# Optimization experiments

Hardware: AMD Instinct MI355X
Metric: run time of the kernel (lower is better)

The kernel has to match this reference:

```python
import jax, jax.numpy as jnp
import numpy as np

KSIZE = 5  # per init_kwargs
NORMALIZATION = "sum"


def setup_inputs() -> dict:
    key = jax.random.key(0)
    k1, k2 = jax.random.split(key)
    kernel = jax.random.normal(k1, (8, KSIZE * KSIZE, 508, 508), dtype=jnp.float32)
    tensor = jax.random.normal(k2, (8, 3, 512, 512), dtype=jnp.float32)
    return {"kernel": kernel, "tensor": tensor}


def _apply_kernels(kernel, tensor, ksize=KSIZE, normalization=NORMALIZATION):
    # kernel: [bs, k*k, kh, kw], tensor: [bs, ci, h, w]
    kh, kw = kernel.shape[2], kernel.shape[3]
    bs, ci, h, w = tensor.shape
    needed = kh + ksize - 1
    if needed > h:
        crop = (needed - h) // 2
        if crop > 0:
            kernel = kernel[:, :, crop:-crop, crop:-crop]
        kh, kw = kernel.shape[2], kernel.shape[3]
    else:
        crop = (h - needed) // 2
        if crop > 0:
            tensor = tensor[:, :, crop:-crop, crop:-crop]
    # Per-pixel dynamic convolution: for each output pixel (i,j),
    # out[b,c,i,j] = sum_{di,dj} kernel[b, di*k+dj, i, j] * tensor[b, c, i+di, j+dj].
    # Loop over the k*k fixed taps (small, static) instead of materializing
    # the [bs, ci, kh, kw, k*k] unfolded tiles the torch code builds.
    weighted = jnp.zeros((bs, ci, kh, kw), dtype=tensor.dtype)
    for di in range(ksize):
        for dj in range(ksize):
            w_tap = kernel[:, di * ksize + dj][:, None]          # [bs,1,kh,kw]
            weighted = weighted + w_tap * tensor[:, :, di:di + kh, dj:dj + kw]
    if normalization == "sum":
        kernel_sum = jnp.sum(kernel, axis=1, keepdims=True)      # [bs,1,kh,kw]
    elif normalization == "l1":
        kernel_sum = jnp.sum(jnp.abs(kernel), axis=1, keepdims=True)
    else:
        kernel_sum = None
    return weighted, kernel_sum


def reference(kernel, tensor):
    return _apply_kernels(kernel, tensor)
```

## Files before the change

### kernel.cpp

```cpp
#include <hip/hip_runtime.h>


constexpr int BS = 8;
constexpr int CI = 3;
constexpr int KH = 508;
constexpr int KW = 508;
constexpr int TH = 512;
constexpr int TW = 512;
constexpr int KSZ = 5;
constexpr int KK = KSZ * KSZ;
constexpr int QPR = KW / 4;
constexpr long long KPLANE = (long long)KH * KW;
constexpr long long WOUT_SIZE = (long long)BS * CI * KPLANE;

__global__ __launch_bounds__(256) void apply_kernels_kern(
    const float* __restrict__ kern,
    const float* __restrict__ tens,
    float* __restrict__ out)
{
    int tid = blockIdx.x * 256 + threadIdx.x;
    if (tid >= BS * KH * QPR) return;
    int q = tid % QPR;
    int t = tid / QPR;
    int y = t % KH;
    int b = t / KH;
    int x = q * 4;

    const float* kbase = kern + (size_t)b * KK * KPLANE + (size_t)y * KW + x;
    const float* tbase = tens + (size_t)b * CI * TH * TW + (size_t)y * TW + x;

    float acc[CI][4] = {};
    float ksum[4] = {};

#pragma unroll
    for (int di = 0; di < KSZ; ++di) {
        float tr[CI][8];
#pragma unroll
        for (int c = 0; c < CI; ++c) {
            const float* tp = tbase + (size_t)c * TH * TW + (size_t)di * TW;
            const float4 a  = *(const float4*)(tp);
            const float4 b4 = *(const float4*)(tp + 4);
            tr[c][0] = a.x;  tr[c][1] = a.y;  tr[c][2] = a.z;  tr[c][3] = a.w;
            tr[c][4] = b4.x; tr[c][5] = b4.y; tr[c][6] = b4.z; tr[c][7] = b4.w;
        }
#pragma unroll
        for (int dj = 0; dj < KSZ; ++dj) {
            const float4 k4 = *(const float4*)(kbase + (size_t)(di * KSZ + dj) * KPLANE);
            const float kv[4] = {k4.x, k4.y, k4.z, k4.w};
#pragma unroll
            for (int l = 0; l < 4; ++l) {
                ksum[l] += kv[l];
#pragma unroll
                for (int c = 0; c < CI; ++c)
                    acc[c][l] += kv[l] * tr[c][l + dj];
            }
        }
    }

#pragma unroll
    for (int c = 0; c < CI; ++c) {
        float4 v = {acc[c][0], acc[c][1], acc[c][2], acc[c][3]};
        *(float4*)(out + ((size_t)(b * CI + c) * KH + y) * KW + x) = v;
    }
    float4 s = {ksum[0], ksum[1], ksum[2], ksum[3]};
    *(float4*)(out + WOUT_SIZE + ((size_t)b * KH + y) * KW + x) = s;
}

extern "C" void kernel_launch(void* const* d_in, const int* in_sizes, int n_in,
                              void* d_out, int out_size, void* d_ws, size_t ws_size,
                              hipStream_t stream) {
    const float* kern = (const float*)d_in[0];
    const float* tens = (const float*)d_in[1];
    float* out = (float*)d_out;
    const int total = BS * KH * QPR;
    const int blocks = (total + 255) / 256;
    apply_kernels_kern<<<blocks, 256, 0, stream>>>(kern, tens, out);
}
```

Measured before the change: 300.8 us.

## Compute two output rows per thread and use nontemporal kernel loads/stores

Each thread now produces outputs for two adjacent rows. It loads six tensor rows instead of ten, so tensor reads are shared across both rows. The per-pixel kernel weights and the outputs, which are streamed once, now go through nontemporal load and store builtins to avoid polluting the cache. This halves the thread count and raises register pressure per thread. The workload is dominated by the kernel-weight stream, which is unchanged in size.

```diff
diff --git a/kernel.cpp b/kernel.cpp
--- a/kernel.cpp
+++ b/kernel.cpp
@@ -10,8 +10,18 @@
 constexpr int KSZ = 5;
 constexpr int KK = KSZ * KSZ;
 constexpr int QPR = KW / 4;
+constexpr int YPAIRS = KH / 2;
 constexpr long long KPLANE = (long long)KH * KW;
 constexpr long long WOUT_SIZE = (long long)BS * CI * KPLANE;
+
+typedef float vf4 __attribute__((ext_vector_type(4)));
+
+__device__ __forceinline__ vf4 nt_load4(const float* p) {
+    return __builtin_nontemporal_load((const vf4*)p);
+}
+__device__ __forceinline__ void nt_store4(float* p, vf4 v) {
+    __builtin_nontemporal_store(v, (vf4*)p);
+}
 
 __global__ __launch_bounds__(256) void apply_kernels_kern(
     const float* __restrict__ kern,
@@ -19,51 +29,61 @@
     float* __restrict__ out)
 {
     int tid = blockIdx.x * 256 + threadIdx.x;
-    if (tid >= BS * KH * QPR) return;
+    if (tid >= BS * YPAIRS * QPR) return;
     int q = tid % QPR;
     int t = tid / QPR;
-    int y = t % KH;
-    int b = t / KH;
+    int yi = t % YPAIRS;
+    int b = t / YPAIRS;
+    int y0 = yi * 2;
     int x = q * 4;
 
-    const float* kbase = kern + (size_t)b * KK * KPLANE + (size_t)y * KW + x;
-    const float* tbase = tens + (size_t)b * CI * TH * TW + (size_t)y * TW + x;
+    const float* kbase = kern + (size_t)b * KK * KPLANE + (size_t)y0 * KW + x;
+    const float* tbase = tens + (size_t)b * CI * TH * TW + (size_t)y0 * TW + x;
 
-    float acc[CI][4] = {};
-    float ksum[4] = {};
+    float acc[2][CI][4] = {};
+    float ksum[2][4] = {};
 
 #pragma unroll
-    for (int di = 0; di < KSZ; ++di) {
-        float tr[CI][8];
+    for (int r = 0; r < KSZ + 1; ++r) {
+        float tw[CI][8];
 #pragma unroll
         for (int c = 0; c < CI; ++c) {
-            const float* tp = tbase + (size_t)c * TH * TW + (size_t)di * TW;
-            const float4 a  = *(const float4*)(tp);
-            const float4 b4 = *(const float4*)(tp + 4);
-            tr[c][0] = a.x;  tr[c][1] = a.y;  tr[c][2] = a.z;  tr[c][3] = a.w;
-            tr[c][4] = b4.x; tr[c][5] = b4.y; tr[c][6] = b4.z; tr[c][7] = b4.w;
+            const float* tp = tbase + (size_t)c * TH * TW + (size_t)r * TW;
+            const vf4 a  = *(const vf4*)(tp);
+            const vf4 b4 = *(const vf4*)(tp + 4);
+            tw[c][0] = a.x;  tw[c][1] = a.y;  tw[c][2] = a.z;  tw[c][3] = a.w;
+            tw[c][4] = b4.x; tw[c][5] = b4.y; tw[c][6] = b4.z; tw[c][7] = b4.w;
         }
 #pragma unroll
-        for (int dj = 0; dj < KSZ; ++dj) {
-            const float4 k4 = *(const float4*)(kbase + (size_t)(di * KSZ + dj) * KPLANE);
-            const float kv[4] = {k4.x, k4.y, k4.z, k4.w};
+        for (int o = 0; o < 2; ++o) {
+            int di = r - o;
+            if (di < 0 || di >= KSZ) continue;
 #pragma unroll
-            for (int l = 0; l < 4; ++l) {
-                ksum[l] += kv[l];
+            for (int dj = 0; dj < KSZ; ++dj) {
+                const vf4 k4 = nt_load4(kbase + (size_t)o * KW +
+                                        (size_t)(di * KSZ + dj) * KPLANE);
+                const float kv[4] = {k4.x, k4.y, k4.z, k4.w};
 #pragma unroll
-                for (int c = 0; c < CI; ++c)
-                    acc[c][l] += kv[l] * tr[c][l + dj];
+                for (int l = 0; l < 4; ++l) {
+                    ksum[o][l] += kv[l];
+#pragma unroll
+                    for (int c = 0; c < CI; ++c)
+                        acc[o][c][l] += kv[l] * tw[c][l + dj];
+                }
             }
         }
     }
 
 #pragma unroll
-    for (int c = 0; c < CI; ++c) {
-        float4 v = {acc[c][0], acc[c][1], acc[c][2], acc[c][3]};
-        *(float4*)(out + ((size_t)(b * CI + c) * KH + y) * KW + x) = v;
+    for (int o = 0; o < 2; ++o) {
+#pragma unroll
+        for (int c = 0; c < CI; ++c) {
+            vf4 v = {acc[o][c][0], acc[o][c][1], acc[o][c][2], acc[o][c][3]};
+            nt_store4(out + ((size_t)(b * CI + c) * KH + (y0 + o)) * KW + x, v);
+        }
+        vf4 s = {ksum[o][0], ksum[o][1], ksum[o][2], ksum[o][3]};
+        nt_store4(out + WOUT_SIZE + ((size_t)b * KH + (y0 + o)) * KW + x, s);
     }
-    float4 s = {ksum[0], ksum[1], ksum[2], ksum[3]};
-    *(float4*)(out + WOUT_SIZE + ((size_t)b * KH + y) * KW + x) = s;
 }
 
 extern "C" void kernel_launch(void* const* d_in, const int* in_sizes, int n_in,
@@ -72,7 +92,7 @@
     const float* kern = (const float*)d_in[0];
     const float* tens = (const float*)d_in[1];
     float* out = (float*)d_out;
-    const int total = BS * KH * QPR;
+    const int total = BS * YPAIRS * QPR;
     const int blocks = (total + 255) / 256;
     apply_kernels_kern<<<blocks, 256, 0, stream>>>(kern, tens, out);
 }
```

After: 297.9 us. Within noise of the previous version (-1.0%).
